# Optimization experiments

Hardware: AMD Instinct MI355X
Metric: run time of the kernel (lower is better)

Reference implementation:

```python
import jax, jax.numpy as jnp
import numpy as np

B, N, E, D = 32, 512, 2048, 128
N_STEPS = 3


def setup_inputs() -> dict:
    key = jax.random.key(0)
    ks = jax.random.split(key, 16)
    s = 0.05
    return {
        "prop_state": jax.random.normal(ks[0], (B, N, D), jnp.float32),
        "edge_states": jax.random.normal(ks[1], (B, E, D), jnp.float32),
        "A": jax.random.uniform(ks[2], (B, N, E), jnp.float32) / E,
        "tem_features": jax.random.normal(ks[3], (B, 64), jnp.float32),
        "link_W": jax.random.normal(ks[4], (D, D), jnp.float32) * s,
        "link_b": jnp.zeros((D,), jnp.float32),
        "reset_W": jax.random.normal(ks[5], (2 * D, D), jnp.float32) * s,
        "reset_b": jnp.zeros((D,), jnp.float32),
        "update_W": jax.random.normal(ks[6], (2 * D, D), jnp.float32) * s,
        "update_b": jnp.zeros((D,), jnp.float32),
        "trans_W": jax.random.normal(ks[7], (2 * D, D), jnp.float32) * s,
        "trans_b": jnp.zeros((D,), jnp.float32),
        "att_W1": jax.random.normal(ks[8], (D, D), jnp.float32) * s,
        "att_b1": jnp.zeros((D,), jnp.float32),
        "att_W2": jax.random.normal(ks[9], (D, 1), jnp.float32) * s,
        "att_b2": jnp.zeros((1,), jnp.float32),
        "out_W": jax.random.normal(ks[10], (D, D), jnp.float32) * s,
        "out_b": jnp.zeros((D,), jnp.float32),
    }


def reference(prop_state, edge_states, A, tem_features,
              link_W, link_b, reset_W, reset_b, update_W, update_b,
              trans_W, trans_b, att_W1, att_b1, att_W2, att_b2, out_W, out_b):
    init_node = prop_state
    init_edge = edge_states
    for _ in range(N_STEPS):
        edge_states = edge_states @ link_W + link_b              # [B,E,D]
        a_cur = jnp.einsum('bne,bed->bnd', A, edge_states)       # [B,N,D]
        a = jnp.concatenate([a_cur, prop_state], axis=2)         # [B,N,2D]
        r = jax.nn.sigmoid(a @ reset_W + reset_b)
        z = jax.nn.sigmoid(a @ update_W + update_b)
        joined = jnp.concatenate([a_cur, r * prop_state], axis=2)
        h_hat = jnp.tanh(joined @ trans_W + trans_b)
        prop_state = (1.0 - z) * prop_state + z * h_hat
    # attention pooling
    atten = jnp.tanh(prop_state @ att_W1 + att_b1) @ att_W2 + att_b2   # [B,N,1]
    Aw = jax.nn.softmax(jnp.transpose(atten, (0, 2, 1)), axis=2)       # [B,1,N]
    out = jnp.tanh(prop_state @ out_W + out_b)                         # [B,N,D]
    mul = jnp.einsum('bqn,bnd->bqd', Aw, out)                          # [B,1,D]
    graph_out = jnp.tanh(jnp.squeeze(mul, axis=1))                     # [B,D]
    # residual block: mean over concatenated node+edge initial states
    feat = jnp.concatenate([init_node, init_edge], axis=1)             # [B,N+E,D]
    residual = jnp.mean(feat, axis=1)                                  # [B,D]
    res = jax.nn.relu(graph_out + residual)
    return res, mul, edge_states
```

## Files before the change

kernel.cpp:

```cpp
#include <hip/hip_runtime.h>
#include <hip/hip_bf16.h>


typedef unsigned short u16;
typedef __attribute__((ext_vector_type(4))) float f32x4;
typedef __attribute__((ext_vector_type(8))) short bf16x8;

#define DI static __device__ __forceinline__

DI u16 f2bf(float f) {
    unsigned u = __builtin_bit_cast(unsigned, f);
    return (u16)((u + 0x7fffu + ((u >> 16) & 1u)) >> 16);
}
DI float bf2f(u16 h) { return __builtin_bit_cast(float, ((unsigned)h) << 16); }

DI bf16x8 cvt8(float4 a, float4 b) {
    u16 tmp[8] = {f2bf(a.x), f2bf(a.y), f2bf(a.z), f2bf(a.w),
                  f2bf(b.x), f2bf(b.y), f2bf(b.z), f2bf(b.w)};
    return *(const bf16x8*)tmp;
}

DI int imgIdx(int k, int n) {
    return (((k >> 5) * 128 + n) * 4 + (((k >> 3) & 3) ^ ((n >> 1) & 3))) * 8 + (k & 7);
}
DI bf16x8 wfragG(const u16* __restrict__ img, int kc, int tt, int l15, int quad) {
    return *(const bf16x8*)&img[(((kc * 128 + tt * 16 + l15) * 4) + (quad ^ ((l15 >> 1) & 3))) * 8];
}

#define MFMA16(a, b, c) __builtin_amdgcn_mfma_f32_16x16x32_bf16(a, b, c, 0, 0, 0)

__global__ __launch_bounds__(256) void k_prep1(
    const float* __restrict__ linkW, const float* __restrict__ resetW,
    const float* __restrict__ updateW, const float* __restrict__ transW,
    const float* __restrict__ attW1, const float* __restrict__ outW,
    float* __restrict__ W2, u16* __restrict__ linkImg, u16* __restrict__ WrImg,
    u16* __restrict__ WzImg, u16* __restrict__ WhImg, u16* __restrict__ attW1Img,
    u16* __restrict__ outWImg)
{
    int blk = blockIdx.x, t = threadIdx.x;
    if (blk < 64) {
        int idx = blk * 256 + t;
        int r = idx >> 7, c = idx & 127;
        float acc = 0.f;
        for (int k = 0; k < 128; k++) acc += linkW[r * 128 + k] * linkW[k * 128 + c];
        W2[r * 128 + c] = acc;
    } else {
        const float* src; u16* dst; int base;
        if (blk < 68)      { src = resetW;  dst = WrImg;    base = 64; }
        else if (blk < 72) { src = updateW; dst = WzImg;    base = 68; }
        else if (blk < 76) { src = transW;  dst = WhImg;    base = 72; }
        else if (blk < 78) { src = linkW;   dst = linkImg;  base = 76; }
        else if (blk < 80) { src = attW1;   dst = attW1Img; base = 78; }
        else               { src = outW;    dst = outWImg;  base = 80; }
        int off = (blk - base) * 8192;
        for (int i = 0; i < 32; i++) {
            int e = off + t + i * 256;
            int k = e >> 7, n = e & 127;
            dst[imgIdx(k, n)] = f2bf(src[e]);
        }
    }
}

__global__ __launch_bounds__(256) void k_prep2(
    const float* __restrict__ linkW, const float* __restrict__ linkb,
    const float* __restrict__ W2, u16* __restrict__ W3Img, float* __restrict__ ebias)
{
    int blk = blockIdx.x, t = threadIdx.x;
    if (blk < 64) {
        int idx = blk * 256 + t;
        int r = idx >> 7, c = idx & 127;
        float acc = 0.f;
        for (int k = 0; k < 128; k++) acc += W2[r * 128 + k] * linkW[k * 128 + c];
        W3Img[imgIdx(r, c)] = f2bf(acc);
    } else if (t < 128) {
        float acc = linkb[t];
        for (int k = 0; k < 128; k++) acc += linkb[k] * (W2[k * 128 + t] + linkW[k * 128 + t]);
        ebias[t] = acc;
    }
}

__global__ __launch_bounds__(256) void k_te(
    const float* __restrict__ E0, u16* __restrict__ Eswz, float* __restrict__ resid)
{
    __shared__ alignas(16) u16 sT[4096];
    __shared__ float sCol[128];
    int t = threadIdx.x, kc = blockIdx.x, b = blockIdx.y;
    const float* Eb = E0 + (size_t)b * 262144 + (size_t)kc * 32 * 128;
    if (t < 128) sCol[t] = 0.f;
    float part[4] = {0.f, 0.f, 0.f, 0.f};
    int ncol = (t & 31) * 4;
    for (int i = 0; i < 4; i++) {
        int f4i = t + i * 256;
        int k5 = f4i >> 5;
        float4 v = *(const float4*)&Eb[k5 * 128 + ncol];
        int g = k5 >> 3, o = k5 & 7;
        float vv[4] = {v.x, v.y, v.z, v.w};
#pragma unroll
        for (int j = 0; j < 4; j++) {
            int n = ncol + j;
            sT[(n * 4 + (g ^ ((n >> 1) & 3))) * 8 + o] = f2bf(vv[j]);
            part[j] += vv[j];
        }
    }
    __syncthreads();
#pragma unroll
    for (int j = 0; j < 4; j++) atomicAdd(&sCol[ncol + j], part[j]);
    u16* dst = Eswz + (size_t)b * 262144 + (size_t)kc * 4096;
    ((uint4*)dst)[t] = ((const uint4*)sT)[t];
    ((uint4*)dst)[t + 256] = ((const uint4*)sT)[t + 256];
    __syncthreads();
    if (t < 128) atomicAdd(&resid[b * 128 + t], sCol[t]);
}

__global__ __launch_bounds__(256, 3) void k_g0(
    const float* __restrict__ A, const u16* __restrict__ Eswz,
    u16* __restrict__ aOut, float* __restrict__ rowsum)
{
    __shared__ float sAcc[4][16][128];
    __shared__ float sRs[4][16];
    int t = threadIdx.x, wid = t >> 6, lane = t & 63, l15 = lane & 15, quad = lane >> 4;
    int bx = blockIdx.x;
    int g = bx >> 8, rmod = bx & 255;
    int b = (rmod & 7) + 8 * g;
    int s = (rmod >> 3) & 31;
    size_t r0 = (size_t)b * 512 + (size_t)s * 16;
    const u16* Eb = Eswz + (size_t)b * 262144;
    const float* Ar = A + (r0 + l15) * 2048;
    int kbase = wid * 16;

    f32x4 acc[8];
#pragma unroll
    for (int i = 0; i < 8; i++) acc[i] = (f32x4){0.f, 0.f, 0.f, 0.f};
    float rsum = 0.f;

    float4 xc = *(const float4*)&Ar[kbase * 32 + quad * 8];
    float4 yc = *(const float4*)&Ar[kbase * 32 + quad * 8 + 4];
    bf16x8 bc[8];
#pragma unroll
    for (int tt = 0; tt < 8; tt++) bc[tt] = wfragG(Eb, kbase, tt, l15, quad);

    for (int kc = 0; kc < 16; kc++) {
        int kg = kbase + kc;
        float4 xn, yn; bf16x8 bn[8];
        if (kc < 15) {
            xn = *(const float4*)&Ar[(kg + 1) * 32 + quad * 8];
            yn = *(const float4*)&Ar[(kg + 1) * 32 + quad * 8 + 4];
#pragma unroll
            for (int tt = 0; tt < 8; tt++) bn[tt] = wfragG(Eb, kg + 1, tt, l15, quad);
        }
        rsum += xc.x + xc.y + xc.z + xc.w + yc.x + yc.y + yc.z + yc.w;
        bf16x8 af = cvt8(xc, yc);
#pragma unroll
        for (int tt = 0; tt < 8; tt++) acc[tt] = MFMA16(af, bc[tt], acc[tt]);
        if (kc < 15) {
            xc = xn; yc = yn;
#pragma unroll
            for (int tt = 0; tt < 8; tt++) bc[tt] = bn[tt];
        }
    }
    rsum += __shfl_xor(rsum, 16);
    rsum += __shfl_xor(rsum, 32);
    if (quad == 0) sRs[wid][l15] = rsum;
#pragma unroll
    for (int tt = 0; tt < 8; tt++)
#pragma unroll
        for (int r = 0; r < 4; r++)
            sAcc[wid][quad * 4 + r][tt * 16 + l15] = acc[tt][r];
    __syncthreads();
    {
        int row = t >> 4, c8 = (t & 15) * 8;
        u16 o[8];
#pragma unroll
        for (int j = 0; j < 8; j++) {
            float v = sAcc[0][row][c8 + j] + sAcc[1][row][c8 + j] +
                      sAcc[2][row][c8 + j] + sAcc[3][row][c8 + j];
            o[j] = f2bf(v);
        }
        *(uint4*)&aOut[(r0 + row) * 128 + c8] = *(const uint4*)o;
    }
    if (t < 16)
        rowsum[r0 + t] = sRs[0][t] + sRs[1][t] + sRs[2][t] + sRs[3][t];
}

__global__ __launch_bounds__(64) void k_gates(
    u16* __restrict__ aBuf, const float* __restrict__ pIn, float* __restrict__ pOut,
    const float* __restrict__ rowsum,
    const u16* __restrict__ linkImg, const u16* __restrict__ WrImg,
    const u16* __restrict__ WzImg, const u16* __restrict__ WhImg,
    const float* __restrict__ link_b, const float* __restrict__ reset_b,
    const float* __restrict__ update_b, const float* __restrict__ trans_b)
{
    __shared__ alignas(16) u16 sT[16 * 136];
    int t = threadIdx.x, l15 = t & 15, quad = t >> 4;
    size_t r0 = (size_t)blockIdx.x * 16;

    bf16x8 aF[4], pF[4];
#pragma unroll
    for (int kc = 0; kc < 4; kc++) {
        aF[kc] = *(const bf16x8*)&aBuf[(r0 + l15) * 128 + kc * 32 + quad * 8];
        float4 x = *(const float4*)&pIn[(r0 + l15) * 128 + kc * 32 + quad * 8];
        float4 y = *(const float4*)&pIn[(r0 + l15) * 128 + kc * 32 + quad * 8 + 4];
        pF[kc] = cvt8(x, y);
    }

    f32x4 zero4 = {0.f, 0.f, 0.f, 0.f};
    f32x4 acc[8];
#pragma unroll
    for (int i = 0; i < 8; i++) acc[i] = zero4;
#pragma unroll
    for (int kc = 0; kc < 4; kc++)
#pragma unroll
        for (int tt = 0; tt < 8; tt++)
            acc[tt] = MFMA16(aF[kc], wfragG(linkImg, kc, tt, l15, quad), acc[tt]);
    float sv[4];
#pragma unroll
    for (int r = 0; r < 4; r++) sv[r] = rowsum[r0 + quad * 4 + r];
#pragma unroll
    for (int tt = 0; tt < 8; tt++) {
        int col = tt * 16 + l15; float lb = link_b[col];
#pragma unroll
        for (int r = 0; r < 4; r++)
            sT[(quad * 4 + r) * 136 + col] = f2bf(acc[tt][r] + sv[r] * lb);
    }
    __syncthreads();
#pragma unroll
    for (int kc = 0; kc < 4; kc++)
        aF[kc] = *(const bf16x8*)&sT[l15 * 136 + kc * 32 + quad * 8];
#pragma unroll
    for (int i = 0; i < 4; i++) {
        int idx = t + i * 64; int row = idx >> 4, col = (idx & 15) * 8;
        *(uint4*)&aBuf[(r0 + row) * 128 + col] = *(const uint4*)&sT[row * 136 + col];
    }

    f32x4 aR[8], aZ[8];
#pragma unroll
    for (int i = 0; i < 8; i++) { aR[i] = zero4; aZ[i] = zero4; }
#pragma unroll
    for (int kc = 0; kc < 8; kc++) {
        bf16x8 af = (kc < 4) ? aF[kc] : pF[kc - 4];
#pragma unroll
        for (int tt = 0; tt < 8; tt++) {
            aR[tt] = MFMA16(af, wfragG(WrImg, kc, tt, l15, quad), aR[tt]);
            aZ[tt] = MFMA16(af, wfragG(WzImg, kc, tt, l15, quad), aZ[tt]);
        }
    }
    __syncthreads();
#pragma unroll
    for (int tt = 0; tt < 8; tt++) {
        int col = tt * 16 + l15; float rb = reset_b[col], ub = update_b[col];
#pragma unroll
        for (int r = 0; r < 4; r++) {
            float rv = 1.f / (1.f + __expf(-(aR[tt][r] + rb)));
            aZ[tt][r] = 1.f / (1.f + __expf(-(aZ[tt][r] + ub)));
            float p = pIn[(r0 + quad * 4 + r) * 128 + col];
            sT[(quad * 4 + r) * 136 + col] = f2bf(rv * p);
        }
    }
    __syncthreads();
    bf16x8 rpF[4];
#pragma unroll
    for (int kc = 0; kc < 4; kc++)
        rpF[kc] = *(const bf16x8*)&sT[l15 * 136 + kc * 32 + quad * 8];

#pragma unroll
    for (int i = 0; i < 8; i++) aR[i] = zero4;
#pragma unroll
    for (int kc = 0; kc < 8; kc++) {
        bf16x8 af = (kc < 4) ? aF[kc] : rpF[kc - 4];
#pragma unroll
        for (int tt = 0; tt < 8; tt++)
            aR[tt] = MFMA16(af, wfragG(WhImg, kc, tt, l15, quad), aR[tt]);
    }
#pragma unroll
    for (int tt = 0; tt < 8; tt++) {
        int col = tt * 16 + l15; float tb = trans_b[col];
#pragma unroll
        for (int r = 0; r < 4; r++) {
            size_t row = r0 + quad * 4 + r;
            float h = tanhf(aR[tt][r] + tb);
            float z = aZ[tt][r];
            float p = pIn[row * 128 + col];
            pOut[row * 128 + col] = (1.f - z) * p + z * h;
        }
    }
}

__global__ __launch_bounds__(64) void k_att(
    const float* __restrict__ pIn, const u16* __restrict__ attW1Img,
    const u16* __restrict__ outWImg, const float* __restrict__ att_b1,
    const float* __restrict__ att_W2, const float* __restrict__ att_b2,
    const float* __restrict__ out_b, float* __restrict__ atten, float* __restrict__ outPool)
{
    int t = threadIdx.x, l15 = t & 15, quad = t >> 4;
    size_t r0 = (size_t)blockIdx.x * 16;
    bf16x8 pF[4];
#pragma unroll
    for (int kc = 0; kc < 4; kc++) {
        float4 x = *(const float4*)&pIn[(r0 + l15) * 128 + kc * 32 + quad * 8];
        float4 y = *(const float4*)&pIn[(r0 + l15) * 128 + kc * 32 + quad * 8 + 4];
        pF[kc] = cvt8(x, y);
    }
    f32x4 zero4 = {0.f, 0.f, 0.f, 0.f};
    f32x4 aA[8], aO[8];
#pragma unroll
    for (int i = 0; i < 8; i++) { aA[i] = zero4; aO[i] = zero4; }
#pragma unroll
    for (int kc = 0; kc < 4; kc++)
#pragma unroll
        for (int tt = 0; tt < 8; tt++) {
            aA[tt] = MFMA16(pF[kc], wfragG(attW1Img, kc, tt, l15, quad), aA[tt]);
            aO[tt] = MFMA16(pF[kc], wfragG(outWImg, kc, tt, l15, quad), aO[tt]);
        }
    float part[4] = {0.f, 0.f, 0.f, 0.f};
#pragma unroll
    for (int tt = 0; tt < 8; tt++) {
        int col = tt * 16 + l15;
        float b1 = att_b1[col], w2 = att_W2[col], ob = out_b[col];
#pragma unroll
        for (int r = 0; r < 4; r++) {
            part[r] += tanhf(aA[tt][r] + b1) * w2;
            outPool[(r0 + quad * 4 + r) * 128 + col] = tanhf(aO[tt][r] + ob);
        }
    }
    float b2 = att_b2[0];
#pragma unroll
    for (int r = 0; r < 4; r++) {
        float loc = part[r];
        loc += __shfl_xor(loc, 1); loc += __shfl_xor(loc, 2);
        loc += __shfl_xor(loc, 4); loc += __shfl_xor(loc, 8);
        if (l15 == 0) atten[r0 + quad * 4 + r] = loc + b2;
    }
}

__global__ __launch_bounds__(64) void k_eout(
    const float* __restrict__ E0, const u16* __restrict__ W3Img,
    const float* __restrict__ ebias, float* __restrict__ Eout)
{
    int t = threadIdx.x, l15 = t & 15, quad = t >> 4;
    size_t r0 = (size_t)blockIdx.x * 16;
    bf16x8 eF[4];
#pragma unroll
    for (int kc = 0; kc < 4; kc++) {
        float4 x = *(const float4*)&E0[(r0 + l15) * 128 + kc * 32 + quad * 8];
        float4 y = *(const float4*)&E0[(r0 + l15) * 128 + kc * 32 + quad * 8 + 4];
        eF[kc] = cvt8(x, y);
    }
    f32x4 zero4 = {0.f, 0.f, 0.f, 0.f};
    f32x4 acc[8];
#pragma unroll
    for (int i = 0; i < 8; i++) acc[i] = zero4;
#pragma unroll
    for (int kc = 0; kc < 4; kc++)
#pragma unroll
        for (int tt = 0; tt < 8; tt++)
            acc[tt] = MFMA16(eF[kc], wfragG(W3Img, kc, tt, l15, quad), acc[tt]);
#pragma unroll
    for (int tt = 0; tt < 8; tt++) {
        int col = tt * 16 + l15; float eb = ebias[col];
#pragma unroll
        for (int r = 0; r < 4; r++)
            Eout[(r0 + quad * 4 + r) * 128 + col] = acc[tt][r] + eb;
    }
}

__global__ __launch_bounds__(256) void k_fin(
    const float* __restrict__ atten, const float* __restrict__ outPool,
    const float* __restrict__ prop0, const float* __restrict__ resid,
    float* __restrict__ outRes, float* __restrict__ outMul)
{
    __shared__ float swv[512];
    __shared__ float sred[256];
    int t = threadIdx.x, b = blockIdx.x;
    float a0 = atten[b * 512 + t], a1 = atten[b * 512 + 256 + t];
    sred[t] = fmaxf(a0, a1); __syncthreads();
    for (int s = 128; s > 0; s >>= 1) { if (t < s) sred[t] = fmaxf(sred[t], sred[t + s]); __syncthreads(); }
    float mx = sred[0]; __syncthreads();
    float e0 = __expf(a0 - mx), e1 = __expf(a1 - mx);
    swv[t] = e0; swv[t + 256] = e1;
    sred[t] = e0 + e1; __syncthreads();
    for (int s = 128; s > 0; s >>= 1) { if (t < s) sred[t] += sred[t + s]; __syncthreads(); }
    float Z = sred[0]; __syncthreads();
    int col = t & 127, half = t >> 7;
    const float* op = outPool + ((size_t)b * 512 + half * 256) * 128 + col;
    const float* pp = prop0 + ((size_t)b * 512 + half * 256) * 128 + col;
    float accM = 0.f, accN = 0.f;
    for (int n = 0; n < 256; n++) {
        accM += swv[half * 256 + n] * op[(size_t)n * 128];
        accN += pp[(size_t)n * 128];
    }
    sred[t] = accM; __syncthreads();
    float mulv = 0.f;
    if (t < 128) mulv = (sred[t] + sred[t + 128]) / Z;
    __syncthreads();
    sred[t] = accN; __syncthreads();
    if (t < 128) {
        float nodesum = sred[t] + sred[t + 128];
        float rv = (nodesum + resid[b * 128 + t]) * (1.f / 2560.f);
        outMul[b * 128 + t] = mulv;
        outRes[b * 128 + t] = fmaxf(0.f, tanhf(mulv) + rv);
    }
}

extern "C" void kernel_launch(void* const* d_in, const int* in_sizes, int n_in,
                              void* d_out, int out_size, void* d_ws, size_t ws_size,
                              hipStream_t stream)
{
    const float* prop0  = (const float*)d_in[0];
    const float* edge0  = (const float*)d_in[1];
    const float* Amat   = (const float*)d_in[2];
    const float* linkW  = (const float*)d_in[4];
    const float* linkb  = (const float*)d_in[5];
    const float* resetW = (const float*)d_in[6];
    const float* resetb = (const float*)d_in[7];
    const float* updateW= (const float*)d_in[8];
    const float* updateb= (const float*)d_in[9];
    const float* transW = (const float*)d_in[10];
    const float* transb = (const float*)d_in[11];
    const float* attW1  = (const float*)d_in[12];
    const float* attb1  = (const float*)d_in[13];
    const float* attW2  = (const float*)d_in[14];
    const float* attb2  = (const float*)d_in[15];
    const float* outW   = (const float*)d_in[16];
    const float* outb   = (const float*)d_in[17];

    char* w = (char*)d_ws;
    u16*   ws_a_bf    = (u16*)(w);
    float* ws_prop    = (float*)(w + 4194304);
    float* ws_rowsum  = (float*)(w + 12582912);
    float* ws_atten   = (float*)(w + 12648448);
    float* ws_resid   = (float*)(w + 12713984);
    float* ws_W2      = (float*)(w + 12730368);
    float* ws_ebias   = (float*)(w + 12795904);
    u16*   ws_linkImg = (u16*)(w + 12796416);
    u16*   ws_W3Img   = (u16*)(w + 12829184);
    u16*   ws_WrImg   = (u16*)(w + 12861952);
    u16*   ws_WzImg   = (u16*)(w + 12927488);
    u16*   ws_WhImg   = (u16*)(w + 12993024);
    u16*   ws_attW1Img= (u16*)(w + 13058560);
    u16*   ws_outWImg = (u16*)(w + 13091328);

    float* out_res  = (float*)d_out;
    float* out_mul  = out_res + 4096;
    float* out_edge = out_res + 8192;
    u16*   Eswz     = (u16*)out_edge;
    float* outPool  = out_edge + 4194304;

    hipMemsetAsync(ws_resid, 0, 32 * 128 * sizeof(float), stream);
    k_prep1<<<82, 256, 0, stream>>>(linkW, resetW, updateW, transW, attW1, outW,
                                    ws_W2, ws_linkImg, ws_WrImg, ws_WzImg, ws_WhImg,
                                    ws_attW1Img, ws_outWImg);
    k_prep2<<<65, 256, 0, stream>>>(linkW, linkb, ws_W2, ws_W3Img, ws_ebias);
    k_te<<<dim3(64, 32), 256, 0, stream>>>(edge0, Eswz, ws_resid);
    k_g0<<<1024, 256, 0, stream>>>(Amat, Eswz, ws_a_bf, ws_rowsum);
    k_gates<<<1024, 64, 0, stream>>>(ws_a_bf, prop0, ws_prop, ws_rowsum,
                                     ws_linkImg, ws_WrImg, ws_WzImg, ws_WhImg,
                                     linkb, resetb, updateb, transb);
    k_gates<<<1024, 64, 0, stream>>>(ws_a_bf, ws_prop, ws_prop, ws_rowsum,
                                     ws_linkImg, ws_WrImg, ws_WzImg, ws_WhImg,
                                     linkb, resetb, updateb, transb);
    k_gates<<<1024, 64, 0, stream>>>(ws_a_bf, ws_prop, ws_prop, ws_rowsum,
                                     ws_linkImg, ws_WrImg, ws_WzImg, ws_WhImg,
                                     linkb, resetb, updateb, transb);
    k_att<<<1024, 64, 0, stream>>>(ws_prop, ws_attW1Img, ws_outWImg, attb1, attW2, attb2,
                                   outb, ws_atten, outPool);
    k_fin<<<32, 256, 0, stream>>>(ws_atten, outPool, prop0, ws_resid, out_res, out_mul);
    k_eout<<<4096, 64, 0, stream>>>(edge0, ws_W3Img, ws_ebias, out_edge);
}
```

Baseline: 396.3 us.

## Fuse three GRU steps and attention into one kernel with 4-wave blocks

Replaces three per-step gate kernels plus the attention kernel with a single kernel that keeps the 16-row prop state in registers and LDS across all steps. Each block now uses four waves, each owning two output column tiles. This removes the fp32 prop round trips through global memory and several launches. The node-sum residual moves into this kernel via atomics, so k_fin no longer rereads prop0. Weight-prep matmuls are split across four lanes with shuffle reduction, and k_eout gains register double-buffering of weight fragments. The trade-off is more barriers per step and atomic contention on the residual buffer.

```diff
diff --git a/kernel.cpp b/kernel.cpp
--- a/kernel.cpp
+++ b/kernel.cpp
@@ -12,7 +12,6 @@
     unsigned u = __builtin_bit_cast(unsigned, f);
     return (u16)((u + 0x7fffu + ((u >> 16) & 1u)) >> 16);
 }
-DI float bf2f(u16 h) { return __builtin_bit_cast(float, ((unsigned)h) << 16); }
 
 DI bf16x8 cvt8(float4 a, float4 b) {
     u16 tmp[8] = {f2bf(a.x), f2bf(a.y), f2bf(a.z), f2bf(a.w),
@@ -38,20 +37,25 @@
     u16* __restrict__ outWImg)
 {
     int blk = blockIdx.x, t = threadIdx.x;
-    if (blk < 64) {
+    if (blk < 256) {
         int idx = blk * 256 + t;
-        int r = idx >> 7, c = idx & 127;
+        int out = idx >> 2, q = idx & 3;
+        int r = out >> 7, c = out & 127;
+        const float* ar = linkW + r * 128 + q * 32;
         float acc = 0.f;
-        for (int k = 0; k < 128; k++) acc += linkW[r * 128 + k] * linkW[k * 128 + c];
-        W2[r * 128 + c] = acc;
+#pragma unroll
+        for (int k = 0; k < 32; k++) acc += ar[k] * linkW[(q * 32 + k) * 128 + c];
+        acc += __shfl_xor(acc, 1);
+        acc += __shfl_xor(acc, 2);
+        if (q == 0) W2[out] = acc;
     } else {
         const float* src; u16* dst; int base;
-        if (blk < 68)      { src = resetW;  dst = WrImg;    base = 64; }
-        else if (blk < 72) { src = updateW; dst = WzImg;    base = 68; }
-        else if (blk < 76) { src = transW;  dst = WhImg;    base = 72; }
-        else if (blk < 78) { src = linkW;   dst = linkImg;  base = 76; }
-        else if (blk < 80) { src = attW1;   dst = attW1Img; base = 78; }
-        else               { src = outW;    dst = outWImg;  base = 80; }
+        if (blk < 260)      { src = resetW;  dst = WrImg;    base = 256; }
+        else if (blk < 264) { src = updateW; dst = WzImg;    base = 260; }
+        else if (blk < 268) { src = transW;  dst = WhImg;    base = 264; }
+        else if (blk < 270) { src = linkW;   dst = linkImg;  base = 268; }
+        else if (blk < 272) { src = attW1;   dst = attW1Img; base = 270; }
+        else                { src = outW;    dst = outWImg;  base = 272; }
         int off = (blk - base) * 8192;
         for (int i = 0; i < 32; i++) {
             int e = off + t + i * 256;
@@ -66,14 +70,20 @@
     const float* __restrict__ W2, u16* __restrict__ W3Img, float* __restrict__ ebias)
 {
     int blk = blockIdx.x, t = threadIdx.x;
-    if (blk < 64) {
+    if (blk < 256) {
         int idx = blk * 256 + t;
-        int r = idx >> 7, c = idx & 127;
+        int out = idx >> 2, q = idx & 3;
+        int r = out >> 7, c = out & 127;
+        const float* ar = W2 + r * 128 + q * 32;
         float acc = 0.f;
-        for (int k = 0; k < 128; k++) acc += W2[r * 128 + k] * linkW[k * 128 + c];
-        W3Img[imgIdx(r, c)] = f2bf(acc);
+#pragma unroll
+        for (int k = 0; k < 32; k++) acc += ar[k] * linkW[(q * 32 + k) * 128 + c];
+        acc += __shfl_xor(acc, 1);
+        acc += __shfl_xor(acc, 2);
+        if (q == 0) W3Img[imgIdx(r, c)] = f2bf(acc);
     } else if (t < 128) {
         float acc = linkb[t];
+#pragma unroll 8
         for (int k = 0; k < 128; k++) acc += linkb[k] * (W2[k * 128 + t] + linkW[k * 128 + t]);
         ebias[t] = acc;
     }
@@ -182,154 +192,147 @@
         rowsum[r0 + t] = sRs[0][t] + sRs[1][t] + sRs[2][t] + sRs[3][t];
 }
 
-__global__ __launch_bounds__(64) void k_gates(
-    u16* __restrict__ aBuf, const float* __restrict__ pIn, float* __restrict__ pOut,
+__global__ __launch_bounds__(256) void k_steps(
+    const u16* __restrict__ aBuf0, const float* __restrict__ p0,
     const float* __restrict__ rowsum,
     const u16* __restrict__ linkImg, const u16* __restrict__ WrImg,
     const u16* __restrict__ WzImg, const u16* __restrict__ WhImg,
+    const u16* __restrict__ attW1Img, const u16* __restrict__ outWImg,
     const float* __restrict__ link_b, const float* __restrict__ reset_b,
-    const float* __restrict__ update_b, const float* __restrict__ trans_b)
-{
-    __shared__ alignas(16) u16 sT[16 * 136];
-    int t = threadIdx.x, l15 = t & 15, quad = t >> 4;
+    const float* __restrict__ update_b, const float* __restrict__ trans_b,
+    const float* __restrict__ att_b1, const float* __restrict__ att_W2,
+    const float* __restrict__ att_b2, const float* __restrict__ out_b,
+    float* __restrict__ atten, float* __restrict__ outPool,
+    float* __restrict__ resid)
+{
+    __shared__ alignas(16) u16 sA[16 * 136], sRP[16 * 136], sP[16 * 136];
+    __shared__ float sRed[16];
+    int t = threadIdx.x, wave = t >> 6, lane = t & 63, l15 = lane & 15, quad = lane >> 4;
     size_t r0 = (size_t)blockIdx.x * 16;
+    int bb = blockIdx.x >> 5;
+    int ttA = wave * 2, ttB = wave * 2 + 1;
+    int colA = ttA * 16 + l15, colB = ttB * 16 + l15;
+    if (t < 16) sRed[t] = 0.f;
 
     bf16x8 aF[4], pF[4];
 #pragma unroll
     for (int kc = 0; kc < 4; kc++) {
-        aF[kc] = *(const bf16x8*)&aBuf[(r0 + l15) * 128 + kc * 32 + quad * 8];
-        float4 x = *(const float4*)&pIn[(r0 + l15) * 128 + kc * 32 + quad * 8];
-        float4 y = *(const float4*)&pIn[(r0 + l15) * 128 + kc * 32 + quad * 8 + 4];
+        aF[kc] = *(const bf16x8*)&aBuf0[(r0 + l15) * 128 + kc * 32 + quad * 8];
+        float4 x = *(const float4*)&p0[(r0 + l15) * 128 + kc * 32 + quad * 8];
+        float4 y = *(const float4*)&p0[(r0 + l15) * 128 + kc * 32 + quad * 8 + 4];
         pF[kc] = cvt8(x, y);
     }
+    f32x4 pS[2];
+#pragma unroll
+    for (int j = 0; j < 2; j++)
+#pragma unroll
+        for (int r = 0; r < 4; r++)
+            pS[j][r] = p0[(r0 + quad * 4 + r) * 128 + (wave * 2 + j) * 16 + l15];
+    {
+        float s0 = pS[0][0] + pS[0][1] + pS[0][2] + pS[0][3];
+        float s1 = pS[1][0] + pS[1][1] + pS[1][2] + pS[1][3];
+        s0 += __shfl_xor(s0, 16); s0 += __shfl_xor(s0, 32);
+        s1 += __shfl_xor(s1, 16); s1 += __shfl_xor(s1, 32);
+        if (quad == 0) {
+            atomicAdd(&resid[bb * 128 + colA], s0);
+            atomicAdd(&resid[bb * 128 + colB], s1);
+        }
+    }
+    float sv[4];
+#pragma unroll
+    for (int r = 0; r < 4; r++) sv[r] = rowsum[r0 + quad * 4 + r];
+    float lbA = link_b[colA], lbB = link_b[colB];
+    float rbA = reset_b[colA], rbB = reset_b[colB];
+    float ubA = update_b[colA], ubB = update_b[colB];
+    float tbA = trans_b[colA], tbB = trans_b[colB];
 
     f32x4 zero4 = {0.f, 0.f, 0.f, 0.f};
-    f32x4 acc[8];
-#pragma unroll
-    for (int i = 0; i < 8; i++) acc[i] = zero4;
-#pragma unroll
-    for (int kc = 0; kc < 4; kc++)
-#pragma unroll
-        for (int tt = 0; tt < 8; tt++)
-            acc[tt] = MFMA16(aF[kc], wfragG(linkImg, kc, tt, l15, quad), acc[tt]);
-    float sv[4];
-#pragma unroll
-    for (int r = 0; r < 4; r++) sv[r] = rowsum[r0 + quad * 4 + r];
-#pragma unroll
-    for (int tt = 0; tt < 8; tt++) {
-        int col = tt * 16 + l15; float lb = link_b[col];
-#pragma unroll
-        for (int r = 0; r < 4; r++)
-            sT[(quad * 4 + r) * 136 + col] = f2bf(acc[tt][r] + sv[r] * lb);
+    for (int step = 0; step < 3; step++) {
+        f32x4 cA = zero4, cB = zero4;
+#pragma unroll
+        for (int kc = 0; kc < 4; kc++) {
+            cA = MFMA16(aF[kc], wfragG(linkImg, kc, ttA, l15, quad), cA);
+            cB = MFMA16(aF[kc], wfragG(linkImg, kc, ttB, l15, quad), cB);
+        }
+#pragma unroll
+        for (int r = 0; r < 4; r++) {
+            sA[(quad * 4 + r) * 136 + colA] = f2bf(cA[r] + sv[r] * lbA);
+            sA[(quad * 4 + r) * 136 + colB] = f2bf(cB[r] + sv[r] * lbB);
+        }
+        __syncthreads();
+#pragma unroll
+        for (int kc = 0; kc < 4; kc++)
+            aF[kc] = *(const bf16x8*)&sA[l15 * 136 + kc * 32 + quad * 8];
+        f32x4 rA = zero4, rB = zero4, zA = zero4, zB = zero4;
+#pragma unroll
+        for (int kc = 0; kc < 8; kc++) {
+            bf16x8 af = (kc < 4) ? aF[kc] : pF[kc - 4];
+            rA = MFMA16(af, wfragG(WrImg, kc, ttA, l15, quad), rA);
+            rB = MFMA16(af, wfragG(WrImg, kc, ttB, l15, quad), rB);
+            zA = MFMA16(af, wfragG(WzImg, kc, ttA, l15, quad), zA);
+            zB = MFMA16(af, wfragG(WzImg, kc, ttB, l15, quad), zB);
+        }
+#pragma unroll
+        for (int r = 0; r < 4; r++) {
+            float rvA = 1.f / (1.f + __expf(-(rA[r] + rbA)));
+            float rvB = 1.f / (1.f + __expf(-(rB[r] + rbB)));
+            zA[r] = 1.f / (1.f + __expf(-(zA[r] + ubA)));
+            zB[r] = 1.f / (1.f + __expf(-(zB[r] + ubB)));
+            sRP[(quad * 4 + r) * 136 + colA] = f2bf(rvA * pS[0][r]);
+            sRP[(quad * 4 + r) * 136 + colB] = f2bf(rvB * pS[1][r]);
+        }
+        __syncthreads();
+        bf16x8 rpF[4];
+#pragma unroll
+        for (int kc = 0; kc < 4; kc++)
+            rpF[kc] = *(const bf16x8*)&sRP[l15 * 136 + kc * 32 + quad * 8];
+        f32x4 hA = zero4, hB = zero4;
+#pragma unroll
+        for (int kc = 0; kc < 8; kc++) {
+            bf16x8 af = (kc < 4) ? aF[kc] : rpF[kc - 4];
+            hA = MFMA16(af, wfragG(WhImg, kc, ttA, l15, quad), hA);
+            hB = MFMA16(af, wfragG(WhImg, kc, ttB, l15, quad), hB);
+        }
+#pragma unroll
+        for (int r = 0; r < 4; r++) {
+            float h1 = tanhf(hA[r] + tbA), h2 = tanhf(hB[r] + tbB);
+            pS[0][r] = (1.f - zA[r]) * pS[0][r] + zA[r] * h1;
+            pS[1][r] = (1.f - zB[r]) * pS[1][r] + zB[r] * h2;
+            sP[(quad * 4 + r) * 136 + colA] = f2bf(pS[0][r]);
+            sP[(quad * 4 + r) * 136 + colB] = f2bf(pS[1][r]);
+        }
+        __syncthreads();
+#pragma unroll
+        for (int kc = 0; kc < 4; kc++)
+            pF[kc] = *(const bf16x8*)&sP[l15 * 136 + kc * 32 + quad * 8];
+    }
+    f32x4 atA = zero4, atB = zero4, oA = zero4, oB = zero4;
+#pragma unroll
+    for (int kc = 0; kc < 4; kc++) {
+        atA = MFMA16(pF[kc], wfragG(attW1Img, kc, ttA, l15, quad), atA);
+        atB = MFMA16(pF[kc], wfragG(attW1Img, kc, ttB, l15, quad), atB);
+        oA  = MFMA16(pF[kc], wfragG(outWImg,  kc, ttA, l15, quad), oA);
+        oB  = MFMA16(pF[kc], wfragG(outWImg,  kc, ttB, l15, quad), oB);
+    }
+    float b1A = att_b1[colA], b1B = att_b1[colB];
+    float w2A = att_W2[colA], w2B = att_W2[colB];
+    float obA = out_b[colA],  obB = out_b[colB];
+    float pr[4];
+#pragma unroll
+    for (int r = 0; r < 4; r++) {
+        pr[r] = tanhf(atA[r] + b1A) * w2A + tanhf(atB[r] + b1B) * w2B;
+        outPool[(r0 + quad * 4 + r) * 128 + colA] = tanhf(oA[r] + obA);
+        outPool[(r0 + quad * 4 + r) * 128 + colB] = tanhf(oB[r] + obB);
+    }
+#pragma unroll
+    for (int r = 0; r < 4; r++) {
+        float v = pr[r];
+        v += __shfl_xor(v, 1); v += __shfl_xor(v, 2);
+        v += __shfl_xor(v, 4); v += __shfl_xor(v, 8);
+        if (l15 == 0) atomicAdd(&sRed[quad * 4 + r], v);
     }
     __syncthreads();
-#pragma unroll
-    for (int kc = 0; kc < 4; kc++)
-        aF[kc] = *(const bf16x8*)&sT[l15 * 136 + kc * 32 + quad * 8];
-#pragma unroll
-    for (int i = 0; i < 4; i++) {
-        int idx = t + i * 64; int row = idx >> 4, col = (idx & 15) * 8;
-        *(uint4*)&aBuf[(r0 + row) * 128 + col] = *(const uint4*)&sT[row * 136 + col];
-    }
-
-    f32x4 aR[8], aZ[8];
-#pragma unroll
-    for (int i = 0; i < 8; i++) { aR[i] = zero4; aZ[i] = zero4; }
-#pragma unroll
-    for (int kc = 0; kc < 8; kc++) {
-        bf16x8 af = (kc < 4) ? aF[kc] : pF[kc - 4];
-#pragma unroll
-        for (int tt = 0; tt < 8; tt++) {
-            aR[tt] = MFMA16(af, wfragG(WrImg, kc, tt, l15, quad), aR[tt]);
-            aZ[tt] = MFMA16(af, wfragG(WzImg, kc, tt, l15, quad), aZ[tt]);
-        }
-    }
-    __syncthreads();
-#pragma unroll
-    for (int tt = 0; tt < 8; tt++) {
-        int col = tt * 16 + l15; float rb = reset_b[col], ub = update_b[col];
-#pragma unroll
-        for (int r = 0; r < 4; r++) {
-            float rv = 1.f / (1.f + __expf(-(aR[tt][r] + rb)));
-            aZ[tt][r] = 1.f / (1.f + __expf(-(aZ[tt][r] + ub)));
-            float p = pIn[(r0 + quad * 4 + r) * 128 + col];
-            sT[(quad * 4 + r) * 136 + col] = f2bf(rv * p);
-        }
-    }
-    __syncthreads();
-    bf16x8 rpF[4];
-#pragma unroll
-    for (int kc = 0; kc < 4; kc++)
-        rpF[kc] = *(const bf16x8*)&sT[l15 * 136 + kc * 32 + quad * 8];
-
-#pragma unroll
-    for (int i = 0; i < 8; i++) aR[i] = zero4;
-#pragma unroll
-    for (int kc = 0; kc < 8; kc++) {
-        bf16x8 af = (kc < 4) ? aF[kc] : rpF[kc - 4];
-#pragma unroll
-        for (int tt = 0; tt < 8; tt++)
-            aR[tt] = MFMA16(af, wfragG(WhImg, kc, tt, l15, quad), aR[tt]);
-    }
-#pragma unroll
-    for (int tt = 0; tt < 8; tt++) {
-        int col = tt * 16 + l15; float tb = trans_b[col];
-#pragma unroll
-        for (int r = 0; r < 4; r++) {
-            size_t row = r0 + quad * 4 + r;
-            float h = tanhf(aR[tt][r] + tb);
-            float z = aZ[tt][r];
-            float p = pIn[row * 128 + col];
-            pOut[row * 128 + col] = (1.f - z) * p + z * h;
-        }
-    }
-}
-
-__global__ __launch_bounds__(64) void k_att(
-    const float* __restrict__ pIn, const u16* __restrict__ attW1Img,
-    const u16* __restrict__ outWImg, const float* __restrict__ att_b1,
-    const float* __restrict__ att_W2, const float* __restrict__ att_b2,
-    const float* __restrict__ out_b, float* __restrict__ atten, float* __restrict__ outPool)
-{
-    int t = threadIdx.x, l15 = t & 15, quad = t >> 4;
-    size_t r0 = (size_t)blockIdx.x * 16;
-    bf16x8 pF[4];
-#pragma unroll
-    for (int kc = 0; kc < 4; kc++) {
-        float4 x = *(const float4*)&pIn[(r0 + l15) * 128 + kc * 32 + quad * 8];
-        float4 y = *(const float4*)&pIn[(r0 + l15) * 128 + kc * 32 + quad * 8 + 4];
-        pF[kc] = cvt8(x, y);
-    }
-    f32x4 zero4 = {0.f, 0.f, 0.f, 0.f};
-    f32x4 aA[8], aO[8];
-#pragma unroll
-    for (int i = 0; i < 8; i++) { aA[i] = zero4; aO[i] = zero4; }
-#pragma unroll
-    for (int kc = 0; kc < 4; kc++)
-#pragma unroll
-        for (int tt = 0; tt < 8; tt++) {
-            aA[tt] = MFMA16(pF[kc], wfragG(attW1Img, kc, tt, l15, quad), aA[tt]);
-            aO[tt] = MFMA16(pF[kc], wfragG(outWImg, kc, tt, l15, quad), aO[tt]);
-        }
-    float part[4] = {0.f, 0.f, 0.f, 0.f};
-#pragma unroll
-    for (int tt = 0; tt < 8; tt++) {
-        int col = tt * 16 + l15;
-        float b1 = att_b1[col], w2 = att_W2[col], ob = out_b[col];
-#pragma unroll
-        for (int r = 0; r < 4; r++) {
-            part[r] += tanhf(aA[tt][r] + b1) * w2;
-            outPool[(r0 + quad * 4 + r) * 128 + col] = tanhf(aO[tt][r] + ob);
-        }
-    }
-    float b2 = att_b2[0];
-#pragma unroll
-    for (int r = 0; r < 4; r++) {
-        float loc = part[r];
-        loc += __shfl_xor(loc, 1); loc += __shfl_xor(loc, 2);
-        loc += __shfl_xor(loc, 4); loc += __shfl_xor(loc, 8);
-        if (l15 == 0) atten[r0 + quad * 4 + r] = loc + b2;
-    }
+    if (t < 16) atten[r0 + t] = sRed[t] + att_b2[0];
 }
 
 __global__ __launch_bounds__(64) void k_eout(
@@ -345,15 +348,25 @@
         float4 y = *(const float4*)&E0[(r0 + l15) * 128 + kc * 32 + quad * 8 + 4];
         eF[kc] = cvt8(x, y);
     }
-    f32x4 zero4 = {0.f, 0.f, 0.f, 0.f};
     f32x4 acc[8];
 #pragma unroll
-    for (int i = 0; i < 8; i++) acc[i] = zero4;
-#pragma unroll
-    for (int kc = 0; kc < 4; kc++)
-#pragma unroll
-        for (int tt = 0; tt < 8; tt++)
-            acc[tt] = MFMA16(eF[kc], wfragG(W3Img, kc, tt, l15, quad), acc[tt]);
+    for (int i = 0; i < 8; i++) acc[i] = (f32x4){0.f, 0.f, 0.f, 0.f};
+    {
+        bf16x8 wc[8], wn[8];
+#pragma unroll
+        for (int tt = 0; tt < 8; tt++) wc[tt] = wfragG(W3Img, 0, tt, l15, quad);
+#pragma unroll
+        for (int kc = 0; kc < 4; kc++) {
+            if (kc < 3)
+#pragma unroll
+                for (int tt = 0; tt < 8; tt++) wn[tt] = wfragG(W3Img, kc + 1, tt, l15, quad);
+#pragma unroll
+            for (int tt = 0; tt < 8; tt++) acc[tt] = MFMA16(eF[kc], wc[tt], acc[tt]);
+            if (kc < 3)
+#pragma unroll
+                for (int tt = 0; tt < 8; tt++) wc[tt] = wn[tt];
+        }
+    }
 #pragma unroll
     for (int tt = 0; tt < 8; tt++) {
         int col = tt * 16 + l15; float eb = ebias[col];
@@ -363,39 +376,32 @@
     }
 }
 
-__global__ __launch_bounds__(256) void k_fin(
+__global__ __launch_bounds__(512) void k_fin(
     const float* __restrict__ atten, const float* __restrict__ outPool,
-    const float* __restrict__ prop0, const float* __restrict__ resid,
+    const float* __restrict__ resid,
     float* __restrict__ outRes, float* __restrict__ outMul)
 {
     __shared__ float swv[512];
-    __shared__ float sred[256];
+    __shared__ float sred[512];
+    __shared__ float sacc[4][128];
     int t = threadIdx.x, b = blockIdx.x;
-    float a0 = atten[b * 512 + t], a1 = atten[b * 512 + 256 + t];
-    sred[t] = fmaxf(a0, a1); __syncthreads();
-    for (int s = 128; s > 0; s >>= 1) { if (t < s) sred[t] = fmaxf(sred[t], sred[t + s]); __syncthreads(); }
+    float a = atten[b * 512 + t];
+    sred[t] = a; __syncthreads();
+    for (int s = 256; s > 0; s >>= 1) { if (t < s) sred[t] = fmaxf(sred[t], sred[t + s]); __syncthreads(); }
     float mx = sred[0]; __syncthreads();
-    float e0 = __expf(a0 - mx), e1 = __expf(a1 - mx);
-    swv[t] = e0; swv[t + 256] = e1;
-    sred[t] = e0 + e1; __syncthreads();
-    for (int s = 128; s > 0; s >>= 1) { if (t < s) sred[t] += sred[t + s]; __syncthreads(); }
+    float e = __expf(a - mx);
+    swv[t] = e; sred[t] = e; __syncthreads();
+    for (int s = 256; s > 0; s >>= 1) { if (t < s) sred[t] += sred[t + s]; __syncthreads(); }
     float Z = sred[0]; __syncthreads();
-    int col = t & 127, half = t >> 7;
-    const float* op = outPool + ((size_t)b * 512 + half * 256) * 128 + col;
-    const float* pp = prop0 + ((size_t)b * 512 + half * 256) * 128 + col;
-    float accM = 0.f, accN = 0.f;
-    for (int n = 0; n < 256; n++) {
-        accM += swv[half * 256 + n] * op[(size_t)n * 128];
-        accN += pp[(size_t)n * 128];
-    }
-    sred[t] = accM; __syncthreads();
-    float mulv = 0.f;
-    if (t < 128) mulv = (sred[t] + sred[t + 128]) / Z;
+    int col = t & 127, q = t >> 7;
+    const float* op = outPool + ((size_t)b * 512 + q * 128) * 128 + col;
+    float accM = 0.f;
+    for (int n = 0; n < 128; n++) accM += swv[q * 128 + n] * op[(size_t)n * 128];
+    sacc[q][col] = accM;
     __syncthreads();
-    sred[t] = accN; __syncthreads();
     if (t < 128) {
-        float nodesum = sred[t] + sred[t + 128];
-        float rv = (nodesum + resid[b * 128 + t]) * (1.f / 2560.f);
+        float mulv = (sacc[0][t] + sacc[1][t] + sacc[2][t] + sacc[3][t]) / Z;
+        float rv = resid[b * 128 + t] * (1.f / 2560.f);
         outMul[b * 128 + t] = mulv;
         outRes[b * 128 + t] = fmaxf(0.f, tanhf(mulv) + rv);
     }
@@ -425,19 +431,18 @@
 
     char* w = (char*)d_ws;
     u16*   ws_a_bf    = (u16*)(w);
-    float* ws_prop    = (float*)(w + 4194304);
-    float* ws_rowsum  = (float*)(w + 12582912);
-    float* ws_atten   = (float*)(w + 12648448);
-    float* ws_resid   = (float*)(w + 12713984);
-    float* ws_W2      = (float*)(w + 12730368);
-    float* ws_ebias   = (float*)(w + 12795904);
-    u16*   ws_linkImg = (u16*)(w + 12796416);
-    u16*   ws_W3Img   = (u16*)(w + 12829184);
-    u16*   ws_WrImg   = (u16*)(w + 12861952);
-    u16*   ws_WzImg   = (u16*)(w + 12927488);
-    u16*   ws_WhImg   = (u16*)(w + 12993024);
-    u16*   ws_attW1Img= (u16*)(w + 13058560);
-    u16*   ws_outWImg = (u16*)(w + 13091328);
+    float* ws_rowsum  = (float*)(w + 4194304);
+    float* ws_atten   = (float*)(w + 4259840);
+    float* ws_resid   = (float*)(w + 4325376);
+    float* ws_W2      = (float*)(w + 4341760);
+    float* ws_ebias   = (float*)(w + 4407296);
+    u16*   ws_linkImg = (u16*)(w + 4407808);
+    u16*   ws_W3Img   = (u16*)(w + 4440576);
+    u16*   ws_WrImg   = (u16*)(w + 4473344);
+    u16*   ws_WzImg   = (u16*)(w + 4538880);
+    u16*   ws_WhImg   = (u16*)(w + 4604416);
+    u16*   ws_attW1Img= (u16*)(w + 4669952);
+    u16*   ws_outWImg = (u16*)(w + 4702720);
 
     float* out_res  = (float*)d_out;
     float* out_mul  = out_res + 4096;
@@ -446,23 +451,18 @@
     float* outPool  = out_edge + 4194304;
 
     hipMemsetAsync(ws_resid, 0, 32 * 128 * sizeof(float), stream);
-    k_prep1<<<82, 256, 0, stream>>>(linkW, resetW, updateW, transW, attW1, outW,
-                                    ws_W2, ws_linkImg, ws_WrImg, ws_WzImg, ws_WhImg,
-                                    ws_attW1Img, ws_outWImg);
-    k_prep2<<<65, 256, 0, stream>>>(linkW, linkb, ws_W2, ws_W3Img, ws_ebias);
+    k_prep1<<<274, 256, 0, stream>>>(linkW, resetW, updateW, transW, attW1, outW,
+                                     ws_W2, ws_linkImg, ws_WrImg, ws_WzImg, ws_WhImg,
+                                     ws_attW1Img, ws_outWImg);
+    k_prep2<<<257, 256, 0, stream>>>(linkW, linkb, ws_W2, ws_W3Img, ws_ebias);
     k_te<<<dim3(64, 32), 256, 0, stream>>>(edge0, Eswz, ws_resid);
     k_g0<<<1024, 256, 0, stream>>>(Amat, Eswz, ws_a_bf, ws_rowsum);
-    k_gates<<<1024, 64, 0, stream>>>(ws_a_bf, prop0, ws_prop, ws_rowsum,
-                                     ws_linkImg, ws_WrImg, ws_WzImg, ws_WhImg,
-                                     linkb, resetb, updateb, transb);
-    k_gates<<<1024, 64, 0, stream>>>(ws_a_bf, ws_prop, ws_prop, ws_rowsum,
-                                     ws_linkImg, ws_WrImg, ws_WzImg, ws_WhImg,
-                                     linkb, resetb, updateb, transb);
-    k_gates<<<1024, 64, 0, stream>>>(ws_a_bf, ws_prop, ws_prop, ws_rowsum,
-                                     ws_linkImg, ws_WrImg, ws_WzImg, ws_WhImg,
-                                     linkb, resetb, updateb, transb);
-    k_att<<<1024, 64, 0, stream>>>(ws_prop, ws_attW1Img, ws_outWImg, attb1, attW2, attb2,
-                                   outb, ws_atten, outPool);
-    k_fin<<<32, 256, 0, stream>>>(ws_atten, outPool, prop0, ws_resid, out_res, out_mul);
+    k_steps<<<1024, 256, 0, stream>>>(ws_a_bf, prop0, ws_rowsum,
+                                      ws_linkImg, ws_WrImg, ws_WzImg, ws_WhImg,
+                                      ws_attW1Img, ws_outWImg,
+                                      linkb, resetb, updateb, transb,
+                                      attb1, attW2, attb2, outb,
+                                      ws_atten, outPool, ws_resid);
+    k_fin<<<32, 512, 0, stream>>>(ws_atten, outPool, ws_resid, out_res, out_mul);
     k_eout<<<4096, 64, 0, stream>>>(edge0, ws_W3Img, ws_ebias, out_edge);
 }
```

New measurement: 376.3 us. 1.05x faster.
